# Kernel tuning notes

Hardware: AMD Instinct MI355X
Metric: run time of the kernel (lower is better)

The kernel has to match this reference:

```python
import jax, jax.numpy as jnp
import numpy as np

DIM = 512
HEADS = 8
EPS = 1e-12  # matches torch F.normalize default eps


def setup_inputs() -> dict:
    key = jax.random.key(0)
    k1, k2, k3, k4 = jax.random.split(key, 4)
    x = jax.random.normal(k1, (4, 2048, DIM), dtype=jnp.float32)
    # nn.Linear(dim, dim*3, bias=False): weight [3*dim, dim], y = x @ W.T
    w_qkv = jax.random.normal(k2, (3 * DIM, DIM), dtype=jnp.float32) * (1.0 / np.sqrt(DIM))
    w_out = jax.random.normal(k3, (DIM, DIM), dtype=jnp.float32) * (1.0 / np.sqrt(DIM))
    temperature = jnp.ones((HEADS, 1, 1), dtype=jnp.float32)
    return {"x": x, "w_qkv": w_qkv, "w_out": w_out, "temperature": temperature}


def _l2norm(t):
    # torch F.normalize(dim=-1): t / max(||t||, eps)
    n = jnp.sqrt(jnp.sum(t * t, axis=-1, keepdims=True))
    return t / jnp.maximum(n, EPS)


def reference(x, w_qkv, w_out, temperature):
    b, n, c = x.shape
    h = HEADS
    d = c // h
    qkv = x @ w_qkv.T  # [b, n, 3c]
    qkv = qkv.reshape(b, n, 3, h, d).transpose(2, 0, 3, 1, 4)  # [3, b, h, n, d]
    q, k, v = qkv[0], qkv[1], qkv[2]
    q = _l2norm(q)
    k = _l2norm(k)
    # cosine attention with learned per-head temperature
    attn = jnp.einsum("bhnd,bhmd->bhnm", q, k) * temperature  # temp broadcasts [h,1,1]
    attn = jax.nn.softmax(attn, axis=-1)
    out = jnp.einsum("bhnm,bhmd->bhnd", attn, v)  # [b, h, n, d]
    out = out.transpose(0, 2, 1, 3).reshape(b, n, c)
    return out @ w_out.T
```

## Files before the change

### kernel.cpp

```cpp
#include <hip/hip_runtime.h>
#include <hip/hip_bf16.h>

using bf16x8 = __attribute__((ext_vector_type(8))) short;
using f32x4  = __attribute__((ext_vector_type(4))) float;
using f32x16 = __attribute__((ext_vector_type(16))) float;
using u32x4  = __attribute__((ext_vector_type(4))) unsigned;

__device__ __forceinline__ short f2bf(float f) {
  union { float f; unsigned u; } v; v.f = f;
  unsigned r = (v.u + 0x7FFFu + ((v.u >> 16) & 1u)) >> 16;
  return (short)(unsigned short)r;
}

__device__ __forceinline__ unsigned cvtpk(float lo, float hi) {
  unsigned r;
  asm("v_cvt_pk_bf16_f32 %0, %1, %2" : "=v"(r) : "v"(lo), "v"(hi));
  return r;
}

__device__ __forceinline__ void plswap(unsigned &a, unsigned &b) {
  asm("v_permlane32_swap_b32 %0, %1" : "+v"(a), "+v"(b));
}

#define GLLDS(gp, lp) __builtin_amdgcn_global_load_lds(                        \
    (const __attribute__((address_space(1))) void*)(gp),                       \
    (__attribute__((address_space(3))) void*)(lp), 16, 0, 0)

__global__ __launch_bounds__(256)
void cvt_f32_bf16(const float* __restrict__ in, short* __restrict__ out, int n8)
{
  int i = blockIdx.x * 256 + threadIdx.x;
  if (i >= n8) return;
  float4 lo = *(const float4*)(in + (size_t)i * 8);
  float4 hi = *(const float4*)(in + (size_t)i * 8 + 4);
  uint4 r;
  r.x = cvtpk(lo.x, lo.y);
  r.y = cvtpk(lo.z, lo.w);
  r.z = cvtpk(hi.x, hi.y);
  r.w = cvtpk(hi.z, hi.w);
  *(uint4*)(out + (size_t)i * 8) = r;
}

__global__ __launch_bounds__(256, 2)
void gemm_qkv(const short* __restrict__ A, const short* __restrict__ B,
              short* __restrict__ outQ, short* __restrict__ outK,
              short* __restrict__ outVt, const float* __restrict__ temp)
{
  __shared__ short As[128 * 32];
  __shared__ short Bs[128 * 32];
  const int Kd = 512;
  const int tid  = threadIdx.x;
  const int lane = tid & 63;
  const int w    = tid >> 6;
  const int wr   = w >> 1, wc = w & 1;
  const int fr   = lane & 15, fq = lane >> 4;
  const int bm = blockIdx.y, bn = blockIdx.x;
  const int rowA = bm * 128, rowB = bn * 128;

  const int lrow   = lane >> 2;
  const int lchunk = ((lane & 3) ^ ((lane >> 3) & 3)) * 8;
  const short* gA0 = A + (size_t)(rowA + w * 32 + lrow) * Kd + lchunk;
  const short* gB0 = B + (size_t)(rowB + w * 32 + lrow) * Kd + lchunk;
  char* lA0 = (char*)As + (w * 32) * 64;
  char* lB0 = (char*)Bs + (w * 32) * 64;
  const int rxor = ((fr >> 1) & 3) << 4;

  f32x4 acc[4][4];
  #pragma unroll
  for (int m = 0; m < 4; ++m)
    #pragma unroll
    for (int n = 0; n < 4; ++n) acc[m][n] = (f32x4){0.f, 0.f, 0.f, 0.f};

  for (int k0 = 0; k0 < Kd; k0 += 32) {
    GLLDS(gA0 + k0,            lA0);
    GLLDS(gA0 + k0 + 16 * Kd,  lA0 + 1024);
    GLLDS(gB0 + k0,            lB0);
    GLLDS(gB0 + k0 + 16 * Kd,  lB0 + 1024);
    __syncthreads();
    bf16x8 afr[4], bfr[4];
    #pragma unroll
    for (int m = 0; m < 4; ++m)
      afr[m] = *(const bf16x8*)((char*)As + (wr*64 + m*16 + fr) * 64 + ((fq*16) ^ rxor));
    #pragma unroll
    for (int n = 0; n < 4; ++n)
      bfr[n] = *(const bf16x8*)((char*)Bs + (wc*64 + n*16 + fr) * 64 + ((fq*16) ^ rxor));
    #pragma unroll
    for (int m = 0; m < 4; ++m)
      #pragma unroll
      for (int n = 0; n < 4; ++n)
        acc[m][n] = __builtin_amdgcn_mfma_f32_16x16x32_bf16(afr[m], bfr[n], acc[m][n], 0, 0, 0);
    __syncthreads();
  }

  const int gc0   = rowB + wc*64;
  const int slice = gc0 >> 6;
  const int t3    = slice >> 3;
  const int h     = slice & 7;
  if (t3 < 2) {
    float scl[4][4];
    const float tval = (t3 == 0) ? temp[h] * 1.44269504088896f : 1.0f;
    #pragma unroll
    for (int m = 0; m < 4; ++m) {
      #pragma unroll
      for (int r = 0; r < 4; ++r) {
        float ss = 0.f;
        #pragma unroll
        for (int n = 0; n < 4; ++n) ss += acc[m][n][r] * acc[m][n][r];
        #pragma unroll
        for (int off = 1; off < 16; off <<= 1) ss += __shfl_xor(ss, off);
        scl[m][r] = tval / fmaxf(sqrtf(ss), 1e-12f);
      }
    }
    short* dst = (t3 == 0) ? outQ : outK;
    #pragma unroll
    for (int m = 0; m < 4; ++m) {
      #pragma unroll
      for (int r = 0; r < 4; ++r) {
        int rg = rowA + wr*64 + m*16 + fq*4 + r;
        int b = rg >> 11, nn = rg & 2047;
        size_t rowoff = ((size_t)(b*8 + h) * 2048 + nn) * 64;
        #pragma unroll
        for (int n = 0; n < 4; ++n)
          dst[rowoff + n*16 + fr] = f2bf(acc[m][n][r] * scl[m][r]);
      }
    }
  } else {
    #pragma unroll
    for (int m = 0; m < 4; ++m) {
      #pragma unroll
      for (int r = 0; r < 4; ++r) {
        int rg = rowA + wr*64 + m*16 + fq*4 + r;
        int b = rg >> 11, nn = rg & 2047;
        #pragma unroll
        for (int n = 0; n < 4; ++n)
          outVt[((size_t)(b*8 + h) * 64 + n*16 + fr) * 2048 + nn] = f2bf(acc[m][n][r]);
      }
    }
  }
}

__global__ __launch_bounds__(256, 2)
void gemm_out(const short* __restrict__ A, const short* __restrict__ B,
              float* __restrict__ outC)
{
  __shared__ short As[128 * 32];
  __shared__ short Bs[128 * 32];
  const int Kd = 512, N = 512;
  const int tid  = threadIdx.x;
  const int lane = tid & 63;
  const int w    = tid >> 6;
  const int wr   = w >> 1, wc = w & 1;
  const int fr   = lane & 15, fq = lane >> 4;
  const int bm = blockIdx.y, bn = blockIdx.x;
  const int rowA = bm * 128, rowB = bn * 128;

  const int lrow   = lane >> 2;
  const int lchunk = ((lane & 3) ^ ((lane >> 3) & 3)) * 8;
  const short* gA0 = A + (size_t)(rowA + w * 32 + lrow) * Kd + lchunk;
  const short* gB0 = B + (size_t)(rowB + w * 32 + lrow) * Kd + lchunk;
  char* lA0 = (char*)As + (w * 32) * 64;
  char* lB0 = (char*)Bs + (w * 32) * 64;
  const int rxor = ((fr >> 1) & 3) << 4;

  f32x4 acc[4][4];
  #pragma unroll
  for (int m = 0; m < 4; ++m)
    #pragma unroll
    for (int n = 0; n < 4; ++n) acc[m][n] = (f32x4){0.f, 0.f, 0.f, 0.f};

  for (int k0 = 0; k0 < Kd; k0 += 32) {
    GLLDS(gA0 + k0,            lA0);
    GLLDS(gA0 + k0 + 16 * Kd,  lA0 + 1024);
    GLLDS(gB0 + k0,            lB0);
    GLLDS(gB0 + k0 + 16 * Kd,  lB0 + 1024);
    __syncthreads();
    bf16x8 afr[4], bfr[4];
    #pragma unroll
    for (int m = 0; m < 4; ++m)
      afr[m] = *(const bf16x8*)((char*)As + (wr*64 + m*16 + fr) * 64 + ((fq*16) ^ rxor));
    #pragma unroll
    for (int n = 0; n < 4; ++n)
      bfr[n] = *(const bf16x8*)((char*)Bs + (wc*64 + n*16 + fr) * 64 + ((fq*16) ^ rxor));
    #pragma unroll
    for (int m = 0; m < 4; ++m)
      #pragma unroll
      for (int n = 0; n < 4; ++n)
        acc[m][n] = __builtin_amdgcn_mfma_f32_16x16x32_bf16(afr[m], bfr[n], acc[m][n], 0, 0, 0);
    __syncthreads();
  }

  #pragma unroll
  for (int m = 0; m < 4; ++m) {
    int r0 = rowA + wr*64 + m*16 + fq*4;
    #pragma unroll
    for (int n = 0; n < 4; ++n) {
      int c = rowB + wc*64 + n*16 + fr;
      #pragma unroll
      for (int r = 0; r < 4; ++r)
        outC[(size_t)(r0 + r) * N + c] = acc[m][n][r];
    }
  }
}

__global__ __launch_bounds__(256, 2)
void attn_fwd(const short* __restrict__ Q, const short* __restrict__ Kt,
              const short* __restrict__ Vt, short* __restrict__ AO,
              const float* __restrict__ temp)
{
  __shared__ short Kl[2][64 * 64];
  __shared__ short Vl[2][64 * 64];
  __shared__ float Ls[4][32];
  const int tid  = threadIdx.x;
  const int lane = tid & 63;
  const int w    = tid >> 6;
  const int l31  = lane & 31;
  const int hi   = lane >> 5;
  const int bh = blockIdx.x;
  const int qt = blockIdx.y;
  const int b = bh >> 3, h = bh & 7;
  const size_t base  = (size_t)bh * 2048 * 64;
  const size_t vbase = (size_t)bh * 64 * 2048;
  const int q0 = qt * 128 + w * 32;

  const short* kp = Kt + base;
  const short* vp = Vt + vbase;

  const int srow  = tid >> 3;
  const int scol8 = (tid & 7) * 8;
  const int scolB = (tid & 7) * 16;
  const int sxor  = (srow & 7) << 4;
  const int kswz  = (l31 & 7) << 4;

  bf16x8 stK[2], stV[2];
  #define LOAD_TILE(T)                                                              \
    do { int kt_ = (T) * 64;                                                        \
      stK[0] = *(const bf16x8*)(kp + (size_t)(kt_ + srow)      * 64 + scol8);       \
      stK[1] = *(const bf16x8*)(kp + (size_t)(kt_ + 32 + srow) * 64 + scol8);       \
      stV[0] = *(const bf16x8*)(vp + (size_t)srow        * 2048 + kt_ + scol8);     \
      stV[1] = *(const bf16x8*)(vp + (size_t)(32 + srow) * 2048 + kt_ + scol8);     \
    } while (0)
  #define WRITE_TILE(P_)                                                            \
    do {                                                                            \
      *(bf16x8*)((char*)Kl[P_] + (srow)      * 128 + (scolB ^ sxor)) = stK[0];      \
      *(bf16x8*)((char*)Kl[P_] + (32 + srow) * 128 + (scolB ^ sxor)) = stK[1];      \
      *(bf16x8*)((char*)Vl[P_] + (srow)      * 128 + (scolB ^ sxor)) = stV[0];      \
      *(bf16x8*)((char*)Vl[P_] + (32 + srow) * 128 + (scolB ^ sxor)) = stV[1];      \
    } while (0)

  bf16x8 bq[4];
  #pragma unroll
  for (int dj = 0; dj < 4; ++dj)
    bq[dj] = *(const bf16x8*)(Q + base + (size_t)(q0 + l31) * 64 + dj*16 + hi*8);

  const float Mh = fabsf(temp[h]) * 1.44269504088896f;
  f32x16 cinit;
  #pragma unroll
  for (int r = 0; r < 16; ++r) cinit[r] = -Mh;

  f32x16 o[2];
  #pragma unroll
  for (int td = 0; td < 2; ++td)
    #pragma unroll
    for (int r = 0; r < 16; ++r) o[td][r] = 0.f;
  float lp = 0.f;

  LOAD_TILE(0); WRITE_TILE(0);
  LOAD_TILE(1); WRITE_TILE(1);
  LOAD_TILE(2);
  __syncthreads();

  for (int t = 0; t < 32; ++t) {
    const int p = t & 1;
    const char* kl = (const char*)Kl[p];
    const char* vl = (const char*)Vl[p];

    f32x16 s[2];
    #pragma unroll
    for (int tk = 0; tk < 2; ++tk) {
      f32x16 z = cinit;
      #pragma unroll
      for (int dj = 0; dj < 4; ++dj) {
        bf16x8 ak = *(const bf16x8*)(kl + (tk*32 + l31) * 128 + ((dj*32 + hi*16) ^ kswz));
        z = __builtin_amdgcn_mfma_f32_32x32x16_bf16(ak, bq[dj], z, 0, 0, 0);
      }
      s[tk] = z;
    }
    #pragma unroll
    for (int tk = 0; tk < 2; ++tk)
      #pragma unroll
      for (int r = 0; r < 16; ++r) {
        float pv = __builtin_amdgcn_exp2f(s[tk][r]);
        s[tk][r] = pv;
        lp += pv;
      }
    bf16x8 pa[4];
    #pragma unroll
    for (int tk = 0; tk < 2; ++tk)
      #pragma unroll
      for (int j = 0; j < 2; ++j) {
        unsigned w0 = cvtpk(s[tk][8*j+0], s[tk][8*j+1]);
        unsigned w2 = cvtpk(s[tk][8*j+4], s[tk][8*j+5]);
        unsigned w1 = cvtpk(s[tk][8*j+2], s[tk][8*j+3]);
        unsigned w3 = cvtpk(s[tk][8*j+6], s[tk][8*j+7]);
        plswap(w0, w2);
        plswap(w1, w3);
        u32x4 pw = {w0, w1, w2, w3};
        pa[tk*2 + j] = __builtin_bit_cast(bf16x8, pw);
      }
    #pragma unroll
    for (int td = 0; td < 2; ++td) {
      f32x16 acc = o[td];
      #pragma unroll
      for (int kj = 0; kj < 4; ++kj) {
        bf16x8 bv = *(const bf16x8*)(vl + (td*32 + l31) * 128 + ((kj*32 + hi*16) ^ kswz));
        acc = __builtin_amdgcn_mfma_f32_32x32x16_bf16(pa[kj], bv, acc, 0, 0, 0);
      }
      o[td] = acc;
    }

    if (t < 31) {
      __syncthreads();
      if (t < 30) {
        WRITE_TILE(p);
        if (t < 29) LOAD_TILE(t + 3);
      }
    }
  }
  #undef LOAD_TILE
  #undef WRITE_TILE

  lp += __shfl_xor(lp, 32);
  if (hi == 0) Ls[w][l31] = 1.0f / lp;
  #pragma unroll
  for (int td = 0; td < 2; ++td)
    #pragma unroll
    for (int r = 0; r < 16; ++r) {
      int qr = (r & 3) + 8 * (r >> 2) + 4 * hi;
      float li = Ls[w][qr];
      int row = b * 2048 + q0 + qr;
      int col = h * 64 + td * 32 + l31;
      AO[(size_t)row * 512 + col] = f2bf(o[td][r] * li);
    }
}

extern "C" void kernel_launch(void* const* d_in, const int* in_sizes, int n_in,
                              void* d_out, int out_size, void* d_ws, size_t ws_size,
                              hipStream_t stream)
{
  const float* x     = (const float*)d_in[0];
  const float* w_qkv = (const float*)d_in[1];
  const float* w_out = (const float*)d_in[2];
  const float* temp  = (const float*)d_in[3];
  float* out = (float*)d_out;
  short* ws  = (short*)d_ws;

  const size_t NQ = (size_t)4 * 8 * 2048 * 64;
  short* Qb   = ws;
  short* Kb   = ws + NQ;
  short* Vtb  = ws + 2 * NQ;
  short* AO16 = ws + 3 * NQ;
  short* xb   = ws + 4 * NQ;
  short* wb   = AO16;
  short* wob  = xb;

  cvt_f32_bf16<<<dim3(2048), 256, 0, stream>>>(x, xb, 524288);
  cvt_f32_bf16<<<dim3(384),  256, 0, stream>>>(w_qkv, wb, 98304);
  gemm_qkv<<<dim3(12, 64), 256, 0, stream>>>(xb, wb, Qb, Kb, Vtb, temp);
  cvt_f32_bf16<<<dim3(128),  256, 0, stream>>>(w_out, wob, 32768);
  attn_fwd<<<dim3(32, 16), 256, 0, stream>>>(Qb, Kb, Vtb, AO16, temp);
  gemm_out<<<dim3(4, 64), 256, 0, stream>>>(AO16, wob, out);
}
```

Measured before the change: 94.48 us.

## Split attention KV across waves with per-wave buffers and LDS reduction; shrink out-GEMM tile

```diff
diff --git a/kernel.cpp b/kernel.cpp
--- a/kernel.cpp
+++ b/kernel.cpp
@@ -144,27 +144,26 @@
               float* __restrict__ outC)
 {
   __shared__ short As[128 * 32];
-  __shared__ short Bs[128 * 32];
+  __shared__ short Bs[64 * 32];
   const int Kd = 512, N = 512;
   const int tid  = threadIdx.x;
   const int lane = tid & 63;
   const int w    = tid >> 6;
-  const int wr   = w >> 1, wc = w & 1;
   const int fr   = lane & 15, fq = lane >> 4;
   const int bm = blockIdx.y, bn = blockIdx.x;
-  const int rowA = bm * 128, rowB = bn * 128;
+  const int rowA = bm * 128, rowB = bn * 64;
 
   const int lrow   = lane >> 2;
   const int lchunk = ((lane & 3) ^ ((lane >> 3) & 3)) * 8;
   const short* gA0 = A + (size_t)(rowA + w * 32 + lrow) * Kd + lchunk;
-  const short* gB0 = B + (size_t)(rowB + w * 32 + lrow) * Kd + lchunk;
+  const short* gB0 = B + (size_t)(rowB + w * 16 + lrow) * Kd + lchunk;
   char* lA0 = (char*)As + (w * 32) * 64;
-  char* lB0 = (char*)Bs + (w * 32) * 64;
+  char* lB0 = (char*)Bs + (w * 16) * 64;
   const int rxor = ((fr >> 1) & 3) << 4;
 
-  f32x4 acc[4][4];
-  #pragma unroll
-  for (int m = 0; m < 4; ++m)
+  f32x4 acc[2][4];
+  #pragma unroll
+  for (int m = 0; m < 2; ++m)
     #pragma unroll
     for (int n = 0; n < 4; ++n) acc[m][n] = (f32x4){0.f, 0.f, 0.f, 0.f};
 
@@ -172,17 +171,16 @@
     GLLDS(gA0 + k0,            lA0);
     GLLDS(gA0 + k0 + 16 * Kd,  lA0 + 1024);
     GLLDS(gB0 + k0,            lB0);
-    GLLDS(gB0 + k0 + 16 * Kd,  lB0 + 1024);
     __syncthreads();
-    bf16x8 afr[4], bfr[4];
-    #pragma unroll
-    for (int m = 0; m < 4; ++m)
-      afr[m] = *(const bf16x8*)((char*)As + (wr*64 + m*16 + fr) * 64 + ((fq*16) ^ rxor));
+    bf16x8 afr[2], bfr[4];
+    #pragma unroll
+    for (int m = 0; m < 2; ++m)
+      afr[m] = *(const bf16x8*)((char*)As + (w*32 + m*16 + fr) * 64 + ((fq*16) ^ rxor));
     #pragma unroll
     for (int n = 0; n < 4; ++n)
-      bfr[n] = *(const bf16x8*)((char*)Bs + (wc*64 + n*16 + fr) * 64 + ((fq*16) ^ rxor));
-    #pragma unroll
-    for (int m = 0; m < 4; ++m)
+      bfr[n] = *(const bf16x8*)((char*)Bs + (n*16 + fr) * 64 + ((fq*16) ^ rxor));
+    #pragma unroll
+    for (int m = 0; m < 2; ++m)
       #pragma unroll
       for (int n = 0; n < 4; ++n)
         acc[m][n] = __builtin_amdgcn_mfma_f32_16x16x32_bf16(afr[m], bfr[n], acc[m][n], 0, 0, 0);
@@ -190,11 +188,11 @@
   }
 
   #pragma unroll
-  for (int m = 0; m < 4; ++m) {
-    int r0 = rowA + wr*64 + m*16 + fq*4;
+  for (int m = 0; m < 2; ++m) {
+    int r0 = rowA + w*32 + m*16 + fq*4;
     #pragma unroll
     for (int n = 0; n < 4; ++n) {
-      int c = rowB + wc*64 + n*16 + fr;
+      int c = rowB + n*16 + fr;
       #pragma unroll
       for (int r = 0; r < 4; ++r)
         outC[(size_t)(r0 + r) * N + c] = acc[m][n][r];
@@ -207,9 +205,8 @@
               const short* __restrict__ Vt, short* __restrict__ AO,
               const float* __restrict__ temp)
 {
-  __shared__ short Kl[2][64 * 64];
-  __shared__ short Vl[2][64 * 64];
-  __shared__ float Ls[4][32];
+  __shared__ short SKV[4 * 2 * 4096];
+  __shared__ float Lsl[4][64];
   const int tid  = threadIdx.x;
   const int lane = tid & 63;
   const int w    = tid >> 6;
@@ -220,127 +217,166 @@
   const int b = bh >> 3, h = bh & 7;
   const size_t base  = (size_t)bh * 2048 * 64;
   const size_t vbase = (size_t)bh * 64 * 2048;
-  const int q0 = qt * 128 + w * 32;
+  const int q0 = qt * 64;
 
   const short* kp = Kt + base;
   const short* vp = Vt + vbase;
 
-  const int srow  = tid >> 3;
-  const int scol8 = (tid & 7) * 8;
-  const int scolB = (tid & 7) * 16;
-  const int sxor  = (srow & 7) << 4;
+  const int swzK  = (((lane & 7) ^ ((lane >> 3) & 7)) << 4);
+  const int vswzW = (((lane & 3) ^ ((lane >> 2) & 3)) << 4);
   const int kswz  = (l31 & 7) << 4;
-
-  bf16x8 stK[2], stV[2];
-  #define LOAD_TILE(T)                                                              \
-    do { int kt_ = (T) * 64;                                                        \
-      stK[0] = *(const bf16x8*)(kp + (size_t)(kt_ + srow)      * 64 + scol8);       \
-      stK[1] = *(const bf16x8*)(kp + (size_t)(kt_ + 32 + srow) * 64 + scol8);       \
-      stV[0] = *(const bf16x8*)(vp + (size_t)srow        * 2048 + kt_ + scol8);     \
-      stV[1] = *(const bf16x8*)(vp + (size_t)(32 + srow) * 2048 + kt_ + scol8);     \
+  const int vswz  = (l31 & 3) << 4;
+
+  char* mybuf0 = (char*)SKV + (w * 2) * 8192;
+
+  bf16x8 sgK[4], sgV[4];
+  #define ISSUE(KT)                                                                 \
+    do { int kb_ = (KT) * 2048;                                                     \
+      _Pragma("unroll")                                                             \
+      for (int i_ = 0; i_ < 4; ++i_)                                                \
+        sgK[i_] = *(const bf16x8*)(kp + kb_ + i_*512 + lane*8);                     \
+      _Pragma("unroll")                                                             \
+      for (int i_ = 0; i_ < 4; ++i_)                                                \
+        sgV[i_] = *(const bf16x8*)(vp + (size_t)(i_*16 + (lane>>2)) * 2048          \
+                                      + (KT)*32 + (lane&3)*8);                      \
     } while (0)
-  #define WRITE_TILE(P_)                                                            \
-    do {                                                                            \
-      *(bf16x8*)((char*)Kl[P_] + (srow)      * 128 + (scolB ^ sxor)) = stK[0];      \
-      *(bf16x8*)((char*)Kl[P_] + (32 + srow) * 128 + (scolB ^ sxor)) = stK[1];      \
-      *(bf16x8*)((char*)Vl[P_] + (srow)      * 128 + (scolB ^ sxor)) = stV[0];      \
-      *(bf16x8*)((char*)Vl[P_] + (32 + srow) * 128 + (scolB ^ sxor)) = stV[1];      \
+  #define WRITEB(P_)                                                                \
+    do { char* b_ = mybuf0 + (P_) * 8192;                                           \
+      _Pragma("unroll")                                                             \
+      for (int i_ = 0; i_ < 4; ++i_)                                                \
+        *(bf16x8*)(b_ + (i_*8 + (lane>>3)) * 128 + swzK) = sgK[i_];                 \
+      _Pragma("unroll")                                                             \
+      for (int i_ = 0; i_ < 4; ++i_)                                                \
+        *(bf16x8*)(b_ + 4096 + (i_*16 + (lane>>2)) * 64 + vswzW) = sgV[i_];         \
     } while (0)
 
-  bf16x8 bq[4];
-  #pragma unroll
-  for (int dj = 0; dj < 4; ++dj)
-    bq[dj] = *(const bf16x8*)(Q + base + (size_t)(q0 + l31) * 64 + dj*16 + hi*8);
+  bf16x8 bq[2][4];
+  #pragma unroll
+  for (int qg = 0; qg < 2; ++qg)
+    #pragma unroll
+    for (int dj = 0; dj < 4; ++dj)
+      bq[qg][dj] = *(const bf16x8*)(Q + base + (size_t)(q0 + qg*32 + l31) * 64 + dj*16 + hi*8);
 
   const float Mh = fabsf(temp[h]) * 1.44269504088896f;
   f32x16 cinit;
   #pragma unroll
   for (int r = 0; r < 16; ++r) cinit[r] = -Mh;
 
-  f32x16 o[2];
-  #pragma unroll
-  for (int td = 0; td < 2; ++td)
-    #pragma unroll
-    for (int r = 0; r < 16; ++r) o[td][r] = 0.f;
-  float lp = 0.f;
-
-  LOAD_TILE(0); WRITE_TILE(0);
-  LOAD_TILE(1); WRITE_TILE(1);
-  LOAD_TILE(2);
+  f32x16 o[2][2];
+  #pragma unroll
+  for (int qg = 0; qg < 2; ++qg)
+    #pragma unroll
+    for (int td = 0; td < 2; ++td)
+      #pragma unroll
+      for (int r = 0; r < 16; ++r) o[qg][td][r] = 0.f;
+  float lp0 = 0.f, lp1 = 0.f;
+
+  ISSUE(w);
+  WRITEB(0);
+  ISSUE(w + 4);
+
+  #pragma unroll 2
+  for (int j = 0; j < 16; ++j) {
+    const int cur = j & 1;
+    if (j < 15) {
+      WRITEB(cur ^ 1);
+      if (j < 14) ISSUE(w + 4 * (j + 2));
+    }
+    const char* kl = mybuf0 + cur * 8192;
+    const char* vl = kl + 4096;
+
+    f32x16 s0 = cinit, s1 = cinit;
+    #pragma unroll
+    for (int dj = 0; dj < 4; ++dj) {
+      bf16x8 ak = *(const bf16x8*)(kl + l31 * 128 + ((dj*32 + hi*16) ^ kswz));
+      s0 = __builtin_amdgcn_mfma_f32_32x32x16_bf16(ak, bq[0][dj], s0, 0, 0, 0);
+      s1 = __builtin_amdgcn_mfma_f32_32x32x16_bf16(ak, bq[1][dj], s1, 0, 0, 0);
+    }
+    #pragma unroll
+    for (int r = 0; r < 16; ++r) {
+      float p0 = __builtin_amdgcn_exp2f(s0[r]);
+      float p1 = __builtin_amdgcn_exp2f(s1[r]);
+      s0[r] = p0; s1[r] = p1;
+      lp0 += p0; lp1 += p1;
+    }
+    bf16x8 pa[2][2];
+    #pragma unroll
+    for (int kj = 0; kj < 2; ++kj) {
+      {
+        unsigned w0 = cvtpk(s0[8*kj+0], s0[8*kj+1]);
+        unsigned w2 = cvtpk(s0[8*kj+4], s0[8*kj+5]);
+        unsigned w1 = cvtpk(s0[8*kj+2], s0[8*kj+3]);
+        unsigned w3 = cvtpk(s0[8*kj+6], s0[8*kj+7]);
+        plswap(w0, w2); plswap(w1, w3);
+        u32x4 pw = {w0, w1, w2, w3};
+        pa[0][kj] = __builtin_bit_cast(bf16x8, pw);
+      }
+      {
+        unsigned w0 = cvtpk(s1[8*kj+0], s1[8*kj+1]);
+        unsigned w2 = cvtpk(s1[8*kj+4], s1[8*kj+5]);
+        unsigned w1 = cvtpk(s1[8*kj+2], s1[8*kj+3]);
+        unsigned w3 = cvtpk(s1[8*kj+6], s1[8*kj+7]);
+        plswap(w0, w2); plswap(w1, w3);
+        u32x4 pw = {w0, w1, w2, w3};
+        pa[1][kj] = __builtin_bit_cast(bf16x8, pw);
+      }
+    }
+    #pragma unroll
+    for (int td = 0; td < 2; ++td)
+      #pragma unroll
+      for (int kj = 0; kj < 2; ++kj) {
+        bf16x8 bv = *(const bf16x8*)(vl + (td*32 + l31) * 64 + ((kj*32 + hi*16) ^ vswz));
+        o[0][td] = __builtin_amdgcn_mfma_f32_32x32x16_bf16(pa[0][kj], bv, o[0][td], 0, 0, 0);
+        o[1][td] = __builtin_amdgcn_mfma_f32_32x32x16_bf16(pa[1][kj], bv, o[1][td], 0, 0, 0);
+      }
+  }
+  #undef ISSUE
+  #undef WRITEB
+
+  lp0 += __shfl_xor(lp0, 32);
+  lp1 += __shfl_xor(lp1, 32);
+  if (hi == 0) {
+    Lsl[w][l31]      = lp0;
+    Lsl[w][32 + l31] = lp1;
+  }
+  float* op = (float*)SKV + w * 4096;
+  #pragma unroll
+  for (int qg = 0; qg < 2; ++qg)
+    #pragma unroll
+    for (int td = 0; td < 2; ++td)
+      #pragma unroll
+      for (int r = 0; r < 16; ++r) {
+        int q = qg*32 + (r & 3) + 8*(r >> 2) + 4*hi;
+        op[q * 64 + td*32 + l31] = o[qg][td][r];
+      }
   __syncthreads();
 
-  for (int t = 0; t < 32; ++t) {
-    const int p = t & 1;
-    const char* kl = (const char*)Kl[p];
-    const char* vl = (const char*)Vl[p];
-
-    f32x16 s[2];
-    #pragma unroll
-    for (int tk = 0; tk < 2; ++tk) {
-      f32x16 z = cinit;
-      #pragma unroll
-      for (int dj = 0; dj < 4; ++dj) {
-        bf16x8 ak = *(const bf16x8*)(kl + (tk*32 + l31) * 128 + ((dj*32 + hi*16) ^ kswz));
-        z = __builtin_amdgcn_mfma_f32_32x32x16_bf16(ak, bq[dj], z, 0, 0, 0);
-      }
-      s[tk] = z;
-    }
-    #pragma unroll
-    for (int tk = 0; tk < 2; ++tk)
-      #pragma unroll
-      for (int r = 0; r < 16; ++r) {
-        float pv = __builtin_amdgcn_exp2f(s[tk][r]);
-        s[tk][r] = pv;
-        lp += pv;
-      }
-    bf16x8 pa[4];
-    #pragma unroll
-    for (int tk = 0; tk < 2; ++tk)
-      #pragma unroll
-      for (int j = 0; j < 2; ++j) {
-        unsigned w0 = cvtpk(s[tk][8*j+0], s[tk][8*j+1]);
-        unsigned w2 = cvtpk(s[tk][8*j+4], s[tk][8*j+5]);
-        unsigned w1 = cvtpk(s[tk][8*j+2], s[tk][8*j+3]);
-        unsigned w3 = cvtpk(s[tk][8*j+6], s[tk][8*j+7]);
-        plswap(w0, w2);
-        plswap(w1, w3);
-        u32x4 pw = {w0, w1, w2, w3};
-        pa[tk*2 + j] = __builtin_bit_cast(bf16x8, pw);
-      }
-    #pragma unroll
-    for (int td = 0; td < 2; ++td) {
-      f32x16 acc = o[td];
-      #pragma unroll
-      for (int kj = 0; kj < 4; ++kj) {
-        bf16x8 bv = *(const bf16x8*)(vl + (td*32 + l31) * 128 + ((kj*32 + hi*16) ^ kswz));
-        acc = __builtin_amdgcn_mfma_f32_32x32x16_bf16(pa[kj], bv, acc, 0, 0, 0);
-      }
-      o[td] = acc;
-    }
-
-    if (t < 31) {
-      __syncthreads();
-      if (t < 30) {
-        WRITE_TILE(p);
-        if (t < 29) LOAD_TILE(t + 3);
-      }
-    }
-  }
-  #undef LOAD_TILE
-  #undef WRITE_TILE
-
-  lp += __shfl_xor(lp, 32);
-  if (hi == 0) Ls[w][l31] = 1.0f / lp;
-  #pragma unroll
-  for (int td = 0; td < 2; ++td)
-    #pragma unroll
-    for (int r = 0; r < 16; ++r) {
-      int qr = (r & 3) + 8 * (r >> 2) + 4 * hi;
-      float li = Ls[w][qr];
-      int row = b * 2048 + q0 + qr;
-      int col = h * 64 + td * 32 + l31;
-      AO[(size_t)row * 512 + col] = f2bf(o[td][r] * li);
-    }
+  {
+    const int q   = tid >> 2;
+    const int d0  = (tid & 3) * 16;
+    const float* ob = (const float*)SKV;
+    f32x4 sum[4];
+    #pragma unroll
+    for (int c = 0; c < 4; ++c) sum[c] = *(const f32x4*)(ob + q*64 + d0 + c*4);
+    #pragma unroll
+    for (int wv = 1; wv < 4; ++wv)
+      #pragma unroll
+      for (int c = 0; c < 4; ++c) {
+        f32x4 t = *(const f32x4*)(ob + wv*4096 + q*64 + d0 + c*4);
+        sum[c] += t;
+      }
+    float linv = 1.0f / (Lsl[0][q] + Lsl[1][q] + Lsl[2][q] + Lsl[3][q]);
+    unsigned pk[8];
+    #pragma unroll
+    for (int c = 0; c < 4; ++c) {
+      pk[c*2]   = cvtpk(sum[c][0] * linv, sum[c][1] * linv);
+      pk[c*2+1] = cvtpk(sum[c][2] * linv, sum[c][3] * linv);
+    }
+    size_t row = (size_t)b * 2048 + q0 + q;
+    short* dst = AO + row * 512 + h * 64 + d0;
+    *(uint4*)(dst)     = make_uint4(pk[0], pk[1], pk[2], pk[3]);
+    *(uint4*)(dst + 8) = make_uint4(pk[4], pk[5], pk[6], pk[7]);
+  }
 }
 
 extern "C" void kernel_launch(void* const* d_in, const int* in_sizes, int n_in,
@@ -367,6 +403,6 @@
   cvt_f32_bf16<<<dim3(384),  256, 0, stream>>>(w_qkv, wb, 98304);
   gemm_qkv<<<dim3(12, 64), 256, 0, stream>>>(xb, wb, Qb, Kb, Vtb, temp);
   cvt_f32_bf16<<<dim3(128),  256, 0, stream>>>(w_out, wob, 32768);
-  attn_fwd<<<dim3(32, 16), 256, 0, stream>>>(Qb, Kb, Vtb, AO16, temp);
-  gemm_out<<<dim3(4, 64), 256, 0, stream>>>(AO16, wob, out);
-}
+  attn_fwd<<<dim3(32, 32), 256, 0, stream>>>(Qb, Kb, Vtb, AO16, temp);
+  gemm_out<<<dim3(8, 64), 256, 0, stream>>>(AO16, wob, out);
+}
```

Measured after the change: 99.45 us. +5.3%, slower.
